# Kernel optimization log

Hardware: AMD Instinct MI355X
Metric: run time of the kernel (lower is better)

The kernel has to match this reference:

```python
import jax, jax.numpy as jnp
import numpy as np

N, E, D, K, H = 100000, 1600000, 32, 3, 1


def setup_inputs() -> dict:
    key = jax.random.key(0)
    ks = jax.random.split(key, 7)
    return {
        "src": jax.random.randint(ks[0], (E,), 0, N),
        "dst": jax.random.randint(ks[1], (E,), 0, N),
        "embedding": jax.random.normal(ks[2], (N, D), jnp.float32),
        "lambda_max": jnp.full((1,), 2.0, jnp.float32),
        # ChebConv: single Linear(k*d -> d) over concatenated Chebyshev terms (shared by both calls)
        "cheb_W": jax.random.normal(ks[3], (K * D, D), jnp.float32) / np.sqrt(K * D),
        "cheb_b": jnp.zeros((D,), jnp.float32),
        # GATv2: fc_src / fc_dst Linear(d -> H*d) + attention vector (H, d)
        "gat_W_src": jax.random.normal(ks[4], (D, H * D), jnp.float32) / np.sqrt(D),
        "gat_b_src": jnp.zeros((H * D,), jnp.float32),
        "gat_W_dst": jax.random.normal(ks[5], (D, H * D), jnp.float32) / np.sqrt(D),
        "gat_b_dst": jnp.zeros((H * D,), jnp.float32),
        "gat_attn": jax.random.normal(ks[6], (H, D), jnp.float32) / np.sqrt(D),
    }


def _cheb(src, dst, feat, lam, W, b, n):
    # DGL ChebConv with lambda_max given; activation = leaky_relu (slope 0.01)
    deg = jnp.clip(jax.ops.segment_sum(jnp.ones(src.shape[0], feat.dtype), dst, num_segments=n), 1.0)
    dinv = deg[:, None] ** -0.5  # D^{-1/2}, (N,1)
    re_norm = 2.0 / lam[0]

    def unnL(f):  # D^{-1/2} A D^{-1/2} f
        return jax.ops.segment_sum((f * dinv)[src], dst, num_segments=n) * dinv

    X0 = feat
    X1 = -re_norm * unnL(X0) + X0 * (re_norm - 1.0)
    Xs = [X0, X1]
    for _ in range(2, K):
        Xi = -2.0 * re_norm * unnL(X1) + X1 * (2.0 * (re_norm - 1.0)) - X0
        Xs.append(Xi)
        X0, X1 = X1, Xi
    return jax.nn.leaky_relu(jnp.concatenate(Xs, axis=1) @ W + b, 0.01)


def _gatv2(src, dst, h, Ws, bs, Wd, bd, attn, n):
    Hh, Dd = attn.shape
    fs = (h @ Ws + bs).reshape(n, Hh, Dd)  # feat_src 'el'
    fd = (h @ Wd + bd).reshape(n, Hh, Dd)  # feat_dst 'er'
    e = jax.nn.leaky_relu(fs[src] + fd[dst], 0.2)        # (E,H,D), GATv2 negative_slope=0.2
    logits = jnp.einsum('ehd,hd->eh', e, attn)           # (E,H)
    m = jax.ops.segment_max(logits, dst, num_segments=n)  # per-dst softmax (edge_softmax)
    ex = jnp.exp(logits - m[dst])
    a = ex / jax.ops.segment_sum(ex, dst, num_segments=n)[dst]
    ft = jax.ops.segment_sum(fs[src] * a[..., None], dst, num_segments=n)  # (N,H,D)
    return jax.nn.leaky_relu(ft, 0.01)  # activation=F.leaky_relu


def reference(src, dst, embedding, lambda_max, cheb_W, cheb_b,
              gat_W_src, gat_b_src, gat_W_dst, gat_b_dst, gat_attn):
    n, d = embedding.shape
    h = _cheb(src, dst, embedding, lambda_max, cheb_W, cheb_b, n)
    h = _cheb(src, dst, h, lambda_max, cheb_W, cheb_b, n)
    out = _gatv2(src, dst, h, gat_W_src, gat_b_src, gat_W_dst, gat_b_dst, gat_attn, n)
    return out.reshape(-1, d)
```

## Files before the change

kernel.cpp:

```cpp
#include <hip/hip_runtime.h>

#define TPB 256
#define NB 512
#define CAPB 4096
#define CHUNK 4096
#define CAPS 5120

__global__ void k_zero_u(unsigned int* p, int n){
  int i = blockIdx.x*TPB + threadIdx.x;
  if(i < n) p[i] = 0u;
}

__global__ void k_scan1(const unsigned int* deg, unsigned int* ptr,
                        unsigned int* bsum, int N){
  __shared__ unsigned int s[TPB];
  int i = blockIdx.x*TPB + threadIdx.x;
  unsigned int v = (i < N) ? deg[i] : 0u;
  s[threadIdx.x] = v; __syncthreads();
  for(int off = 1; off < TPB; off <<= 1){
    unsigned int x = (threadIdx.x >= off) ? s[threadIdx.x - off] : 0u;
    __syncthreads();
    s[threadIdx.x] += x;
    __syncthreads();
  }
  if(i < N) ptr[i] = s[threadIdx.x] - v;
  if(threadIdx.x == TPB-1) bsum[blockIdx.x] = s[TPB-1];
}

__global__ void k_scan2(unsigned int* bsum, int nb){
  __shared__ unsigned int s[TPB];
  __shared__ unsigned int carry;
  if(threadIdx.x == 0) carry = 0u;
  __syncthreads();
  for(int base = 0; base < nb; base += TPB){
    int i = base + threadIdx.x;
    unsigned int v = (i < nb) ? bsum[i] : 0u;
    s[threadIdx.x] = v; __syncthreads();
    for(int off = 1; off < TPB; off <<= 1){
      unsigned int x = (threadIdx.x >= off) ? s[threadIdx.x - off] : 0u;
      __syncthreads();
      s[threadIdx.x] += x;
      __syncthreads();
    }
    if(i < nb) bsum[i] = s[threadIdx.x] - v + carry;
    __syncthreads();
    if(threadIdx.x == 0) carry += s[TPB-1];
    __syncthreads();
  }
}

__global__ void k_scan3(unsigned int* ptr, const unsigned int* bsum, int N, int E){
  int i = blockIdx.x*TPB + threadIdx.x;
  if(i < N) ptr[i] += bsum[blockIdx.x];
  if(i == 0) ptr[N] = (unsigned int)E;
}

__global__ __launch_bounds__(TPB) void k_bin1(const int* src, const int* dst,
    unsigned int* btail, int2* binned, int E, int npb){
  __shared__ unsigned int hist[NB];
  __shared__ unsigned int base[NB];
  int t = threadIdx.x;
  for(int i = t; i < NB; i += TPB) hist[i] = 0u;
  __syncthreads();
  int e0 = blockIdx.x*CHUNK;
  int e1 = e0 + CHUNK; if(e1 > E) e1 = E;
  for(int e = e0 + t; e < e1; e += TPB)
    atomicAdd(&hist[dst[e]/npb], 1u);
  __syncthreads();
  for(int i = t; i < NB; i += TPB){
    unsigned int c = hist[i];
    base[i] = c ? atomicAdd(btail + i, c) : 0u;
    hist[i] = 0u;
  }
  __syncthreads();
  for(int e = e0 + t; e < e1; e += TPB){
    int d = dst[e];
    int b = d / npb;
    unsigned int off = base[b] + atomicAdd(&hist[b], 1u);
    if(off < CAPB) binned[(size_t)b*CAPB + off] = make_int2(src[e], d);
  }
}

__global__ __launch_bounds__(TPB) void k_cnt(const int2* binned, const unsigned int* btail,
    unsigned int* deg, float* dinv, int npb, int N){
  __shared__ unsigned int c[TPB];
  int b = blockIdx.x;
  int n0 = b*npb;
  int t = threadIdx.x;
  c[t] = 0u;
  __syncthreads();
  unsigned int cnt = btail[b]; if(cnt > (unsigned)CAPB) cnt = CAPB;
  const int2* eb = binned + (size_t)b*CAPB;
  for(unsigned int i = t; i < cnt; i += TPB)
    atomicAdd(&c[eb[i].y - n0], 1u);
  __syncthreads();
  int n = n0 + t;
  if(t < npb && n < N){
    unsigned int d = c[t];
    deg[n] = d;
    dinv[n] = 1.0f / sqrtf(fmaxf((float)d, 1.0f));
  }
}

__global__ __launch_bounds__(TPB) void k_bin2(const int2* binned,
    const unsigned int* ptr, int* csr, int npb, int N){
  __shared__ unsigned int curs[256];
  __shared__ int stage[CAPS];
  int b = blockIdx.x;
  int n0 = b*npb; if(n0 >= N) return;
  int n1 = n0 + npb; if(n1 > N) n1 = N;
  int t = threadIdx.x;
  unsigned int segbase = ptr[n0];
  unsigned int seglen  = ptr[n1] - segbase;
  for(int i = n0 + t; i < n1; i += TPB) curs[i - n0] = ptr[i] - segbase;
  __syncthreads();
  unsigned int cnt = seglen < (unsigned)CAPB ? seglen : (unsigned)CAPB;
  const int2* eb = binned + (size_t)b*CAPB;
  if(seglen <= (unsigned)CAPS){
    for(unsigned int i = t; i < cnt; i += TPB){
      int2 sd = eb[i];
      unsigned int p0 = atomicAdd(&curs[sd.y - n0], 1u);
      stage[p0] = sd.x;
    }
    __syncthreads();
    for(unsigned int i = t; i < seglen; i += TPB) csr[segbase + i] = stage[i];
  } else {
    for(unsigned int i = t; i < cnt; i += TPB){
      int2 sd = eb[i];
      unsigned int p0 = atomicAdd(&curs[sd.y - n0], 1u);
      csr[segbase + p0] = sd.x;
    }
  }
}

__device__ __forceinline__ float4 agg_gather4(const unsigned int* ptr, const int* csr,
    const float* X, const float* dinv, int t, int lane){
  int g  = lane >> 3;
  int f4 = (lane & 7) << 2;
  unsigned int p0 = ptr[t], p1 = ptr[t+1];
  float4 S0 = make_float4(0.f,0.f,0.f,0.f);
  float4 S1 = make_float4(0.f,0.f,0.f,0.f);
  for(unsigned int base = p0; base < p1; base += 32){
    int idx = 0; float dva = 0.f;
    unsigned int pos = base + (unsigned)lane;
    if(pos < p1){ idx = csr[pos]; dva = dinv[idx]; }
    unsigned int cnt = p1 - base; if(cnt > 32u) cnt = 32u;
    unsigned int rounds = (cnt + 3u) >> 2;
    for(unsigned int r = 0; r < rounds; r += 2){
      int el0 = (int)(r << 2) + g;
      int s0  = __shfl(idx, el0, 32);
      float d0 = __shfl(dva, el0, 32);
      const float4 x0 = *(const float4*)(X + (size_t)s0*32 + f4);
      if(r + 1 < rounds){
        int el1 = el0 + 4;
        int s1  = __shfl(idx, el1, 32);
        float d1 = __shfl(dva, el1, 32);
        const float4 x1 = *(const float4*)(X + (size_t)s1*32 + f4);
        S1.x += x1.x*d1; S1.y += x1.y*d1; S1.z += x1.z*d1; S1.w += x1.w*d1;
      }
      S0.x += x0.x*d0; S0.y += x0.y*d0; S0.z += x0.z*d0; S0.w += x0.w*d0;
    }
  }
  float4 S;
  S.x = S0.x + S1.x; S.y = S0.y + S1.y; S.z = S0.z + S1.z; S.w = S0.w + S1.w;
  S.x += __shfl_xor(S.x, 8, 32);  S.y += __shfl_xor(S.y, 8, 32);
  S.z += __shfl_xor(S.z, 8, 32);  S.w += __shfl_xor(S.w, 8, 32);
  S.x += __shfl_xor(S.x, 16, 32); S.y += __shfl_xor(S.y, 16, 32);
  S.z += __shfl_xor(S.z, 16, 32); S.w += __shfl_xor(S.w, 16, 32);
  return S;
}

__global__ __launch_bounds__(TPB) void k_cheb1(const unsigned int* ptr, const int* csr,
    const float* X0, const float* dinv, const float* lam, float* X1, int N){
  int t = blockIdx.x*8 + (threadIdx.x >> 5);
  if(t >= N) return;
  int lane = threadIdx.x & 31;
  float4 S = agg_gather4(ptr, csr, X0, dinv, t, lane);
  if((lane >> 3) != 0) return;
  int f4 = (lane & 7) << 2;
  float re = 2.0f / lam[0];
  float dt = dinv[t];
  size_t o = (size_t)t*32 + f4;
  const float4 x0 = *(const float4*)(X0 + o);
  float4 r;
  r.x = -re*(S.x*dt) + (re-1.0f)*x0.x;
  r.y = -re*(S.y*dt) + (re-1.0f)*x0.y;
  r.z = -re*(S.z*dt) + (re-1.0f)*x0.z;
  r.w = -re*(S.w*dt) + (re-1.0f)*x0.w;
  *(float4*)(X1 + o) = r;
}

__global__ __launch_bounds__(TPB) void k_cheb2(const unsigned int* ptr, const int* csr,
    const float* X0, const float* X1, const float* dinv, const float* lam,
    float* X2, int N){
  int t = blockIdx.x*8 + (threadIdx.x >> 5);
  if(t >= N) return;
  int lane = threadIdx.x & 31;
  float4 S = agg_gather4(ptr, csr, X1, dinv, t, lane);
  if((lane >> 3) != 0) return;
  int f4 = (lane & 7) << 2;
  float re = 2.0f / lam[0];
  float dt = dinv[t];
  size_t o = (size_t)t*32 + f4;
  const float4 x0 = *(const float4*)(X0 + o);
  const float4 x1 = *(const float4*)(X1 + o);
  float c1 = -2.0f*re, c2 = 2.0f*(re-1.0f);
  float4 r;
  r.x = c1*(S.x*dt) + c2*x1.x - x0.x;
  r.y = c1*(S.y*dt) + c2*x1.y - x0.y;
  r.z = c1*(S.z*dt) + c2*x1.z - x0.z;
  r.w = c1*(S.w*dt) + c2*x1.w - x0.w;
  *(float4*)(X2 + o) = r;
}

__global__ __launch_bounds__(TPB) void k_cheb_lin(const float* X0, const float* X1,
    const float* X2, const float* W, const float* b, float* out, int N){
  __shared__ float Ws[96*32];
  __shared__ float bs[32];
  int t = threadIdx.x;
  for(int i = t; i < 96*32; i += TPB) Ws[i] = W[i];
  if(t < 32) bs[t] = b[t];
  __syncthreads();
  int n = blockIdx.x*8 + (t >> 5);
  if(n >= N) return;
  int c = t & 31;
  const float* x0 = X0 + (size_t)n*32;
  const float* x1 = X1 + (size_t)n*32;
  const float* x2 = X2 + (size_t)n*32;
  float a = bs[c];
  #pragma unroll
  for(int k = 0; k < 32; k++) a += x0[k]*Ws[k*32+c];
  #pragma unroll
  for(int k = 0; k < 32; k++) a += x1[k]*Ws[(32+k)*32+c];
  #pragma unroll
  for(int k = 0; k < 32; k++) a += x2[k]*Ws[(64+k)*32+c];
  out[(size_t)n*32+c] = a > 0.f ? a : 0.01f*a;
}

__global__ __launch_bounds__(TPB) void k_gat_fc(const float* h,
    const float* Wsr, const float* bsr, const float* Wds, const float* bds,
    float* fs, float* fd, int N){
  __shared__ float ws[1024], wd[1024], b1[32], b2[32];
  int t = threadIdx.x;
  for(int i = t; i < 1024; i += TPB){ ws[i] = Wsr[i]; wd[i] = Wds[i]; }
  if(t < 32){ b1[t] = bsr[t]; b2[t] = bds[t]; }
  __syncthreads();
  int n = blockIdx.x*8 + (t >> 5);
  if(n >= N) return;
  int c = t & 31;
  const float* hr = h + (size_t)n*32;
  float a1 = b1[c], a2 = b2[c];
  #pragma unroll
  for(int k = 0; k < 32; k++){ float hv = hr[k]; a1 += hv*ws[k*32+c]; a2 += hv*wd[k*32+c]; }
  fs[(size_t)n*32+c] = a1;
  fd[(size_t)n*32+c] = a2;
}

__global__ __launch_bounds__(TPB) void k_gat(const unsigned int* ptr, const int* csr,
    const float* fs, const float* fd, const float* attn, float* out, int N){
  int t = blockIdx.x*8 + (threadIdx.x >> 5);
  if(t >= N) return;
  int lane = threadIdx.x & 31;
  int g  = lane >> 3;
  int f4 = (lane & 7) << 2;
  unsigned int p0 = ptr[t], p1 = ptr[t+1];
  const float4 fd4 = *(const float4*)(fd + (size_t)t*32 + f4);
  const float4 at4 = *(const float4*)(attn + f4);
  float m = -3.402823466e38f, den = 0.f;
  float4 acc = make_float4(0.f,0.f,0.f,0.f);
  for(unsigned int base = p0; base < p1; base += 32){
    int idx = 0;
    unsigned int pos = base + (unsigned)lane;
    if(pos < p1) idx = csr[pos];
    unsigned int cnt = p1 - base; if(cnt > 32u) cnt = 32u;
    unsigned int rounds = (cnt + 3u) >> 2;
    for(unsigned int r = 0; r < rounds; r++){
      int el = (int)(r << 2) + g;
      int s  = __shfl(idx, el, 32);
      const float4 f = *(const float4*)(fs + (size_t)s*32 + f4);
      float vx = f.x + fd4.x; vx = vx > 0.f ? vx : 0.2f*vx;
      float vy = f.y + fd4.y; vy = vy > 0.f ? vy : 0.2f*vy;
      float vz = f.z + fd4.z; vz = vz > 0.f ? vz : 0.2f*vz;
      float vw = f.w + fd4.w; vw = vw > 0.f ? vw : 0.2f*vw;
      float pl = vx*at4.x + vy*at4.y + vz*at4.z + vw*at4.w;
      pl += __shfl_xor(pl, 4, 32);
      pl += __shfl_xor(pl, 2, 32);
      pl += __shfl_xor(pl, 1, 32);
      if(el < (int)cnt){
        float mn = fmaxf(m, pl);
        float sc = __expf(m - mn);
        float e  = __expf(pl - mn);
        den = den*sc + e;
        acc.x = acc.x*sc + f.x*e;
        acc.y = acc.y*sc + f.y*e;
        acc.z = acc.z*sc + f.z*e;
        acc.w = acc.w*sc + f.w*e;
        m = mn;
      }
    }
  }
  #pragma unroll
  for(int off = 8; off <= 16; off <<= 1){
    float mo = __shfl_xor(m, off, 32);
    float do_ = __shfl_xor(den, off, 32);
    float ax = __shfl_xor(acc.x, off, 32);
    float ay = __shfl_xor(acc.y, off, 32);
    float az = __shfl_xor(acc.z, off, 32);
    float aw = __shfl_xor(acc.w, off, 32);
    float mn = fmaxf(m, mo);
    float a = __expf(m - mn), b = __expf(mo - mn);
    den = den*a + do_*b;
    acc.x = acc.x*a + ax*b;
    acc.y = acc.y*a + ay*b;
    acc.z = acc.z*a + az*b;
    acc.w = acc.w*a + aw*b;
    m = mn;
  }
  if(g != 0) return;
  float4 o = make_float4(0.f,0.f,0.f,0.f);
  if(den > 0.f){
    float inv = 1.0f / den;
    o.x = acc.x*inv; o.x = o.x > 0.f ? o.x : 0.01f*o.x;
    o.y = acc.y*inv; o.y = o.y > 0.f ? o.y : 0.01f*o.y;
    o.z = acc.z*inv; o.z = o.z > 0.f ? o.z : 0.01f*o.z;
    o.w = acc.w*inv; o.w = o.w > 0.f ? o.w : 0.01f*o.w;
  }
  *(float4*)(out + (size_t)t*32 + f4) = o;
}

extern "C" void kernel_launch(void* const* d_in, const int* in_sizes, int n_in,
                              void* d_out, int out_size, void* d_ws, size_t ws_size,
                              hipStream_t stream){
  const int*   src = (const int*)d_in[0];
  const int*   dst = (const int*)d_in[1];
  const float* emb = (const float*)d_in[2];
  const float* lam = (const float*)d_in[3];
  const float* cW  = (const float*)d_in[4];
  const float* cB  = (const float*)d_in[5];
  const float* gWs = (const float*)d_in[6];
  const float* gbs = (const float*)d_in[7];
  const float* gWd = (const float*)d_in[8];
  const float* gbd = (const float*)d_in[9];
  const float* gat = (const float*)d_in[10];
  const int E  = in_sizes[0];
  const int N  = in_sizes[2] / 32;
  const int NF = N * 32;
  const int npb = (N + NB - 1) / NB;

  int gN  = (N + TPB-1)/TPB;
  int gR  = (N + 7)/8;
  int gB1 = (E + CHUNK-1)/CHUNK;

  char* p = (char*)d_ws;
  auto alloc = [&](size_t bytes)->char*{ char* r = p; p += (bytes + 255) & ~(size_t)255; return r; };
  unsigned int* degi = (unsigned int*)alloc((size_t)N*4);
  unsigned int* ptrA = (unsigned int*)alloc((size_t)(N+1)*4);
  unsigned int* btail= (unsigned int*)alloc((size_t)NB*4);
  unsigned int* bsum = (unsigned int*)alloc((size_t)(gN+1)*4);
  float* dinv = (float*)alloc((size_t)N*4);
  int*   csr  = (int*)alloc((size_t)E*4);
  float* X1   = (float*)alloc((size_t)NF*4);
  float* X2   = (float*)alloc((size_t)NF*4);
  float* h1   = (float*)alloc((size_t)NF*4);
  float* h2   = (float*)alloc((size_t)NF*4);
  int2* binned = (int2*)X1;

  k_zero_u<<<(NB+TPB-1)/TPB, TPB, 0, stream>>>(btail, NB);
  k_bin1<<<gB1, TPB, 0, stream>>>(src, dst, btail, binned, E, npb);
  k_cnt<<<NB, TPB, 0, stream>>>(binned, btail, degi, dinv, npb, N);
  k_scan1<<<gN, TPB, 0, stream>>>(degi, ptrA, bsum, N);
  k_scan2<<<1,  TPB, 0, stream>>>(bsum, gN);
  k_scan3<<<gN, TPB, 0, stream>>>(ptrA, bsum, N, E);
  k_bin2<<<NB,  TPB, 0, stream>>>(binned, ptrA, csr, npb, N);

  k_cheb1<<<gR, TPB, 0, stream>>>(ptrA, csr, emb, dinv, lam, X1, N);
  k_cheb2<<<gR, TPB, 0, stream>>>(ptrA, csr, emb, X1, dinv, lam, X2, N);
  k_cheb_lin<<<gR, TPB, 0, stream>>>(emb, X1, X2, cW, cB, h1, N);

  k_cheb1<<<gR, TPB, 0, stream>>>(ptrA, csr, h1, dinv, lam, X1, N);
  k_cheb2<<<gR, TPB, 0, stream>>>(ptrA, csr, h1, X1, dinv, lam, X2, N);
  k_cheb_lin<<<gR, TPB, 0, stream>>>(h1, X1, X2, cW, cB, h2, N);

  k_gat_fc<<<gR, TPB, 0, stream>>>(h2, gWs, gbs, gWd, gbd, X1 , X2 , N);
  k_gat<<<gR, TPB, 0, stream>>>(ptrA, csr, X1, X2, gat, (float*)d_out, N);
}
```

Measured before the change: 434.0 us.

## Fuse Chebyshev second step with linear layer and GAT projections

Merges the second Chebyshev recurrence, the concatenated linear layer with leaky-relu, and, for the second layer, the GATv2 source and destination projections into one kernel per layer. Row vectors are passed between lanes with shuffles instead of being written to and re-read from global memory. Each block now handles 32 nodes over 4 iterations so the weight load into shared memory is amortised. This removes the X2 and h2 round trips and two or three launches per layer, in exchange for more shared memory and registers per block, which may lower occupancy in the gather-bound aggregation.

Result: slower. 445.8 us (+2.7%).

```diff
diff --git a/kernel.cpp b/kernel.cpp
--- a/kernel.cpp
+++ b/kernel.cpp
@@ -190,70 +190,126 @@
   *(float4*)(X1 + o) = r;
 }
 
-__global__ __launch_bounds__(TPB) void k_cheb2(const unsigned int* ptr, const int* csr,
+#define BCAST4(vec, j) { bx = __shfl(vec.x, j, 32); by = __shfl(vec.y, j, 32); \
+                         bz = __shfl(vec.z, j, 32); bw = __shfl(vec.w, j, 32); }
+
+__global__ __launch_bounds__(TPB) void k_cheb2lin(const unsigned int* ptr, const int* csr,
     const float* X0, const float* X1, const float* dinv, const float* lam,
-    float* X2, int N){
-  int t = blockIdx.x*8 + (threadIdx.x >> 5);
-  if(t >= N) return;
-  int lane = threadIdx.x & 31;
-  float4 S = agg_gather4(ptr, csr, X1, dinv, t, lane);
-  if((lane >> 3) != 0) return;
+    const float* W, const float* b, float* out, int N){
+  __shared__ float Ws[96*32];
+  __shared__ float bs[32];
+  int tid = threadIdx.x;
+  for(int i = tid; i < 96*32; i += TPB) Ws[i] = W[i];
+  if(tid < 32) bs[tid] = b[tid];
+  __syncthreads();
+  int lane = tid & 31;
+  int hw = tid >> 5;
   int f4 = (lane & 7) << 2;
   float re = 2.0f / lam[0];
-  float dt = dinv[t];
-  size_t o = (size_t)t*32 + f4;
-  const float4 x0 = *(const float4*)(X0 + o);
-  const float4 x1 = *(const float4*)(X1 + o);
   float c1 = -2.0f*re, c2 = 2.0f*(re-1.0f);
-  float4 r;
-  r.x = c1*(S.x*dt) + c2*x1.x - x0.x;
-  r.y = c1*(S.y*dt) + c2*x1.y - x0.y;
-  r.z = c1*(S.z*dt) + c2*x1.z - x0.z;
-  r.w = c1*(S.w*dt) + c2*x1.w - x0.w;
-  *(float4*)(X2 + o) = r;
-}
-
-__global__ __launch_bounds__(TPB) void k_cheb_lin(const float* X0, const float* X1,
-    const float* X2, const float* W, const float* b, float* out, int N){
+  for(int it = 0; it < 4; it++){
+    int t = blockIdx.x*32 + it*8 + hw;
+    if(t >= N) continue;
+    float4 S = agg_gather4(ptr, csr, X1, dinv, t, lane);
+    float dt = dinv[t];
+    size_t o = (size_t)t*32 + f4;
+    const float4 x0 = *(const float4*)(X0 + o);
+    const float4 x1 = *(const float4*)(X1 + o);
+    float4 x2;
+    x2.x = c1*(S.x*dt) + c2*x1.x - x0.x;
+    x2.y = c1*(S.y*dt) + c2*x1.y - x0.y;
+    x2.z = c1*(S.z*dt) + c2*x1.z - x0.z;
+    x2.w = c1*(S.w*dt) + c2*x1.w - x0.w;
+    float aA = bs[lane], aB = 0.f;
+    float bx, by, bz, bw;
+    #pragma unroll
+    for(int j = 0; j < 8; j++){
+      BCAST4(x0, j);
+      aA += bx*Ws[(4*j+0)*32+lane]; aB += by*Ws[(4*j+1)*32+lane];
+      aA += bz*Ws[(4*j+2)*32+lane]; aB += bw*Ws[(4*j+3)*32+lane];
+    }
+    #pragma unroll
+    for(int j = 0; j < 8; j++){
+      BCAST4(x1, j);
+      aA += bx*Ws[(32+4*j+0)*32+lane]; aB += by*Ws[(32+4*j+1)*32+lane];
+      aA += bz*Ws[(32+4*j+2)*32+lane]; aB += bw*Ws[(32+4*j+3)*32+lane];
+    }
+    #pragma unroll
+    for(int j = 0; j < 8; j++){
+      BCAST4(x2, j);
+      aA += bx*Ws[(64+4*j+0)*32+lane]; aB += by*Ws[(64+4*j+1)*32+lane];
+      aA += bz*Ws[(64+4*j+2)*32+lane]; aB += bw*Ws[(64+4*j+3)*32+lane];
+    }
+    float a = aA + aB;
+    out[(size_t)t*32 + lane] = a > 0.f ? a : 0.01f*a;
+  }
+}
+
+__global__ __launch_bounds__(TPB) void k_cheb2linfc(const unsigned int* ptr, const int* csr,
+    const float* X0, const float* X1, const float* dinv, const float* lam,
+    const float* W, const float* b,
+    const float* Wsr, const float* bsr, const float* Wds, const float* bds,
+    float* fs, float* fd, int N){
   __shared__ float Ws[96*32];
   __shared__ float bs[32];
-  int t = threadIdx.x;
-  for(int i = t; i < 96*32; i += TPB) Ws[i] = W[i];
-  if(t < 32) bs[t] = b[t];
-  __syncthreads();
-  int n = blockIdx.x*8 + (t >> 5);
-  if(n >= N) return;
-  int c = t & 31;
-  const float* x0 = X0 + (size_t)n*32;
-  const float* x1 = X1 + (size_t)n*32;
-  const float* x2 = X2 + (size_t)n*32;
-  float a = bs[c];
-  #pragma unroll
-  for(int k = 0; k < 32; k++) a += x0[k]*Ws[k*32+c];
-  #pragma unroll
-  for(int k = 0; k < 32; k++) a += x1[k]*Ws[(32+k)*32+c];
-  #pragma unroll
-  for(int k = 0; k < 32; k++) a += x2[k]*Ws[(64+k)*32+c];
-  out[(size_t)n*32+c] = a > 0.f ? a : 0.01f*a;
-}
-
-__global__ __launch_bounds__(TPB) void k_gat_fc(const float* h,
-    const float* Wsr, const float* bsr, const float* Wds, const float* bds,
-    float* fs, float* fd, int N){
   __shared__ float ws[1024], wd[1024], b1[32], b2[32];
-  int t = threadIdx.x;
-  for(int i = t; i < 1024; i += TPB){ ws[i] = Wsr[i]; wd[i] = Wds[i]; }
-  if(t < 32){ b1[t] = bsr[t]; b2[t] = bds[t]; }
-  __syncthreads();
-  int n = blockIdx.x*8 + (t >> 5);
-  if(n >= N) return;
-  int c = t & 31;
-  const float* hr = h + (size_t)n*32;
-  float a1 = b1[c], a2 = b2[c];
-  #pragma unroll
-  for(int k = 0; k < 32; k++){ float hv = hr[k]; a1 += hv*ws[k*32+c]; a2 += hv*wd[k*32+c]; }
-  fs[(size_t)n*32+c] = a1;
-  fd[(size_t)n*32+c] = a2;
+  int tid = threadIdx.x;
+  for(int i = tid; i < 96*32; i += TPB) Ws[i] = W[i];
+  for(int i = tid; i < 1024; i += TPB){ ws[i] = Wsr[i]; wd[i] = Wds[i]; }
+  if(tid < 32){ bs[tid] = b[tid]; b1[tid] = bsr[tid]; b2[tid] = bds[tid]; }
+  __syncthreads();
+  int lane = tid & 31;
+  int hw = tid >> 5;
+  int f4 = (lane & 7) << 2;
+  float re = 2.0f / lam[0];
+  float c1 = -2.0f*re, c2 = 2.0f*(re-1.0f);
+  for(int it = 0; it < 4; it++){
+    int t = blockIdx.x*32 + it*8 + hw;
+    if(t >= N) continue;
+    float4 S = agg_gather4(ptr, csr, X1, dinv, t, lane);
+    float dt = dinv[t];
+    size_t o = (size_t)t*32 + f4;
+    const float4 x0 = *(const float4*)(X0 + o);
+    const float4 x1 = *(const float4*)(X1 + o);
+    float4 x2;
+    x2.x = c1*(S.x*dt) + c2*x1.x - x0.x;
+    x2.y = c1*(S.y*dt) + c2*x1.y - x0.y;
+    x2.z = c1*(S.z*dt) + c2*x1.z - x0.z;
+    x2.w = c1*(S.w*dt) + c2*x1.w - x0.w;
+    float aA = bs[lane], aB = 0.f;
+    float bx, by, bz, bw;
+    #pragma unroll
+    for(int j = 0; j < 8; j++){
+      BCAST4(x0, j);
+      aA += bx*Ws[(4*j+0)*32+lane]; aB += by*Ws[(4*j+1)*32+lane];
+      aA += bz*Ws[(4*j+2)*32+lane]; aB += bw*Ws[(4*j+3)*32+lane];
+    }
+    #pragma unroll
+    for(int j = 0; j < 8; j++){
+      BCAST4(x1, j);
+      aA += bx*Ws[(32+4*j+0)*32+lane]; aB += by*Ws[(32+4*j+1)*32+lane];
+      aA += bz*Ws[(32+4*j+2)*32+lane]; aB += bw*Ws[(32+4*j+3)*32+lane];
+    }
+    #pragma unroll
+    for(int j = 0; j < 8; j++){
+      BCAST4(x2, j);
+      aA += bx*Ws[(64+4*j+0)*32+lane]; aB += by*Ws[(64+4*j+1)*32+lane];
+      aA += bz*Ws[(64+4*j+2)*32+lane]; aB += bw*Ws[(64+4*j+3)*32+lane];
+    }
+    float a = aA + aB;
+    float hv = a > 0.f ? a : 0.01f*a;
+    float s1 = b1[lane], s2 = b2[lane];
+    float s1b = 0.f, s2b = 0.f;
+    #pragma unroll
+    for(int k = 0; k < 32; k += 2){
+      float h0 = __shfl(hv, k,   32);
+      float h1 = __shfl(hv, k+1, 32);
+      s1  += h0*ws[k*32+lane];      s2  += h0*wd[k*32+lane];
+      s1b += h1*ws[(k+1)*32+lane];  s2b += h1*wd[(k+1)*32+lane];
+    }
+    fs[(size_t)t*32 + lane] = s1 + s1b;
+    fd[(size_t)t*32 + lane] = s2 + s2b;
+  }
 }
 
 __global__ __launch_bounds__(TPB) void k_gat(const unsigned int* ptr, const int* csr,
@@ -349,6 +405,7 @@
 
   int gN  = (N + TPB-1)/TPB;
   int gR  = (N + 7)/8;
+  int gF  = (N + 31)/32;
   int gB1 = (E + CHUNK-1)/CHUNK;
 
   char* p = (char*)d_ws;
@@ -360,9 +417,9 @@
   float* dinv = (float*)alloc((size_t)N*4);
   int*   csr  = (int*)alloc((size_t)E*4);
   float* X1   = (float*)alloc((size_t)NF*4);
-  float* X2   = (float*)alloc((size_t)NF*4);
+  float* fs   = (float*)alloc((size_t)NF*4);
+  float* fd   = (float*)alloc((size_t)NF*4);
   float* h1   = (float*)alloc((size_t)NF*4);
-  float* h2   = (float*)alloc((size_t)NF*4);
   int2* binned = (int2*)X1;
 
   k_zero_u<<<(NB+TPB-1)/TPB, TPB, 0, stream>>>(btail, NB);
@@ -374,13 +431,11 @@
   k_bin2<<<NB,  TPB, 0, stream>>>(binned, ptrA, csr, npb, N);
 
   k_cheb1<<<gR, TPB, 0, stream>>>(ptrA, csr, emb, dinv, lam, X1, N);
-  k_cheb2<<<gR, TPB, 0, stream>>>(ptrA, csr, emb, X1, dinv, lam, X2, N);
-  k_cheb_lin<<<gR, TPB, 0, stream>>>(emb, X1, X2, cW, cB, h1, N);
+  k_cheb2lin<<<gF, TPB, 0, stream>>>(ptrA, csr, emb, X1, dinv, lam, cW, cB, h1, N);
 
   k_cheb1<<<gR, TPB, 0, stream>>>(ptrA, csr, h1, dinv, lam, X1, N);
-  k_cheb2<<<gR, TPB, 0, stream>>>(ptrA, csr, h1, X1, dinv, lam, X2, N);
-  k_cheb_lin<<<gR, TPB, 0, stream>>>(h1, X1, X2, cW, cB, h2, N);
-
-  k_gat_fc<<<gR, TPB, 0, stream>>>(h2, gWs, gbs, gWd, gbd, X1 , X2 , N);
-  k_gat<<<gR, TPB, 0, stream>>>(ptrA, csr, X1, X2, gat, (float*)d_out, N);
-}
+  k_cheb2linfc<<<gF, TPB, 0, stream>>>(ptrA, csr, h1, X1, dinv, lam, cW, cB,
+                                       gWs, gbs, gWd, gbd, fs, fd, N);
+
+  k_gat<<<gR, TPB, 0, stream>>>(ptrA, csr, fs, fd, gat, (float*)d_out, N);
+}
```
